# Kernel optimization log

Hardware: AMD Instinct MI355X
Metric: run time of the kernel (lower is better)

Reference implementation:

```python
import jax, jax.numpy as jnp
import numpy as np

N, E, G = 20000, 320000, 128
H, TE, CD = 128, 128, 64
HEADS, DH = 4, 32          # inner = 128 == H
L = 6


def _fwd(p, edge_index, batch):
    """Faithful forward of CrystalDiffusionModel (eval mode: dropout = identity).
    EquivariantGraphConv (imported in the original) is implemented as the standard
    edge-conditioned message-passing conv: m_ij = silu(W[h_src; h_dst; e_ij] + b),
    agg = scatter_add over dst, h' = W_u[h; agg] + b_u."""
    x, ea, t = p['x'], p['edge_attr'], p['t']
    n = x.shape[0]
    h = x @ p['Wn'] + p['bn']                      # [N,H] node embedding
    ef = ea @ p['We'] + p['be']                    # [E,H] edge embedding

    # sinusoidal time embedding -> MLP
    half = TE // 2
    freq = jnp.exp(-jnp.arange(half, dtype=jnp.float32) * (np.log(10000.0) / (half - 1)))
    te = t[:, None] * freq[None, :]
    te = jnp.concatenate([jnp.sin(te), jnp.cos(te)], axis=-1)          # [G,TE]
    te = jax.nn.silu(te @ p['tm_W1'] + p['tm_b1']) @ p['tm_W2'] + p['tm_b2']

    def mlp2(z, W1, b1, W2, b2):
        return jax.nn.silu(z @ W1 + b1) @ W2 + b2

    topo_e = mlp2(p['topo_cond'], p['topo_W1'], p['topo_b1'], p['topo_W2'], p['topo_b2'])
    stab_e = mlp2(p['stab_cond'], p['stab_W1'], p['stab_b1'], p['stab_W2'], p['stab_b2'])
    sust_e = mlp2(p['sust_cond'], p['sust_W1'], p['sust_b1'], p['sust_W2'], p['sust_b2'])
    cond = mlp2(jnp.concatenate([topo_e, stab_e, sust_e], axis=-1),
                p['comb_W1'], p['comb_b1'], p['comb_W2'], p['comb_b2'])  # [G,CD]

    ctx = cond[batch]                               # [N,CD] per-node condition
    # context is a single token per query -> k,v constant across layers
    k = (ctx @ p['Wk']).reshape(n, HEADS, DH)
    v = (ctx @ p['Wv']).reshape(n, HEADS, DH)
    ti = jax.nn.silu(te)[batch]                     # [N,H] time influence (dropout=id)

    src, dst = edge_index[0], edge_index[1]
    scale = DH ** -0.5
    for i in range(L):
        Wm, bm = p['gnn_Wm'][i], p['gnn_bm'][i]
        # split concat-GEMM to avoid materializing [E, 3H]
        m = jax.nn.silu(h[src] @ Wm[:H] + h[dst] @ Wm[H:2 * H] + ef @ Wm[2 * H:] + bm)
        agg = jax.ops.segment_sum(m, dst, num_segments=n)               # [N,H]
        Wu, bu = p['gnn_Wu'][i], p['gnn_bu'][i]
        hu = h @ Wu[:H] + agg @ Wu[H:] + bu
        # LayerNorm
        mu = hu.mean(-1, keepdims=True)
        var = hu.var(-1, keepdims=True)
        hu = (hu - mu) * jax.lax.rsqrt(var + 1e-5) * p['ln_g'][i] + p['ln_b'][i]
        # cross-attention; context length is 1 so softmax over j is exactly 1
        q = (hu @ p['Wq']).reshape(n, HEADS, DH)
        sim = jnp.einsum('nhd,nhd->nh', q, k) * scale                   # [N,heads]
        attn = jax.nn.softmax(sim[..., None], axis=-1)                  # == 1.0
        out = (attn * v).reshape(n, HEADS * DH)
        hu = out @ p['Wo'] + p['bo']
        h = h + hu + ti                              # residual + time influence

    node_pred = jax.nn.silu(h @ p['np_W1'] + p['np_b1']) @ p['np_W2'] + p['np_b2']
    pos_pred = jax.nn.silu(h @ p['pp_W1'] + p['pp_b1']) @ p['pp_W2'] + p['pp_b2']
    return node_pred, pos_pred


def setup_inputs() -> dict:
    key = jax.random.key(0)
    it = iter(jax.random.split(key, 96))

    def nrm(shape, s=0.02):
        return jax.random.normal(next(it), shape, jnp.float32) * s

    z = lambda *s: jnp.zeros(s, jnp.float32)
    inp = {
        'x': jax.random.normal(next(it), (N, 12), jnp.float32),
        'edge_index': jax.random.randint(next(it), (2, E), 0, N),
        'edge_attr': jax.random.normal(next(it), (E, 20), jnp.float32),
        'pos': jax.random.normal(next(it), (N, 3), jnp.float32),
        't': jax.random.uniform(next(it), (G,), jnp.float32) * 1000.0,
        'topo_cond': jax.random.normal(next(it), (G, 7), jnp.float32),
        'stab_cond': jax.random.normal(next(it), (G, 2), jnp.float32),
        'sust_cond': jax.random.normal(next(it), (G, 3), jnp.float32),
        'batch': jnp.sort(jax.random.randint(next(it), (N,), 0, G)),
        'Wn': nrm((12, H)), 'bn': z(H), 'We': nrm((20, H)), 'be': z(H),
        'tm_W1': nrm((TE, 2 * TE)), 'tm_b1': z(2 * TE), 'tm_W2': nrm((2 * TE, TE)), 'tm_b2': z(TE),
        'topo_W1': nrm((7, 32)), 'topo_b1': z(32), 'topo_W2': nrm((32, 32)), 'topo_b2': z(32),
        'stab_W1': nrm((2, 16)), 'stab_b1': z(16), 'stab_W2': nrm((16, 16)), 'stab_b2': z(16),
        'sust_W1': nrm((3, 16)), 'sust_b1': z(16), 'sust_W2': nrm((16, 16)), 'sust_b2': z(16),
        'comb_W1': nrm((64, CD)), 'comb_b1': z(CD), 'comb_W2': nrm((CD, CD)), 'comb_b2': z(CD),
        'Wq': nrm((H, HEADS * DH)), 'Wk': nrm((CD, HEADS * DH)), 'Wv': nrm((CD, HEADS * DH)),
        'Wo': nrm((HEADS * DH, H)), 'bo': z(H),
        'gnn_Wm': nrm((L, 3 * H, H)), 'gnn_bm': z(L, H),
        'gnn_Wu': nrm((L, 2 * H, H)), 'gnn_bu': z(L, H),
        'ln_g': jnp.ones((L, H), jnp.float32), 'ln_b': z(L, H),
        'np_W1': nrm((H, 2 * H)), 'np_b1': z(2 * H), 'np_W2': nrm((2 * H, 12)), 'np_b2': z(12),
        'pp_W1': nrm((H, H)), 'pp_b1': z(H), 'pp_W2': nrm((H, 3)), 'pp_b2': z(3),
    }
    return inp


def reference(x, edge_index, edge_attr, pos, t, topo_cond, stab_cond, sust_cond, batch,
              Wn, bn, We, be, tm_W1, tm_b1, tm_W2, tm_b2,
              topo_W1, topo_b1, topo_W2, topo_b2, stab_W1, stab_b1, stab_W2, stab_b2,
              sust_W1, sust_b1, sust_W2, sust_b2, comb_W1, comb_b1, comb_W2, comb_b2,
              Wq, Wk, Wv, Wo, bo, gnn_Wm, gnn_bm, gnn_Wu, gnn_bu, ln_g, ln_b,
              np_W1, np_b1, np_W2, np_b2, pp_W1, pp_b1, pp_W2, pp_b2):
    loc = dict(locals())
    p = {k: v for k, v in loc.items() if k not in ('edge_index', 'batch', 'pos')}
    return _fwd(p, edge_index, batch)
```

## Files before the change

kernel.cpp:

```cpp
#include <hip/hip_runtime.h>
#include <hip/hip_bf16.h>

#define NN 20000
#define GG 128

typedef __bf16 bf16x8_t __attribute__((ext_vector_type(8)));
typedef float  f32x4_t  __attribute__((ext_vector_type(4)));
typedef __hip_bfloat16 hbf16;

#define PK_NPW1 0
#define PK_PPW1 32768
#define PK_NPW2 49152
#define PK_PPW2 53248
#define PK_WN   55296
#define GADD_OFF 59392

__device__ __forceinline__ float silu_f(float v) {
    return v * __builtin_amdgcn_rcpf(1.0f + __expf(-v));
}

__device__ __forceinline__ void cp_async(hbf16* dst, const hbf16* src,
                                         int nbytes, int w, int lane) {
    const int per_wave = nbytes >> 2;
    const char* g = (const char*)src + w * per_wave + lane * 16;
    char* l = (char*)dst + w * per_wave + lane * 16;
    for (int j = 0; j < per_wave; j += 1024)
        __builtin_amdgcn_global_load_lds(
            (__attribute__((address_space(1))) void*)(g + j),
            (__attribute__((address_space(3))) void*)(l + j),
            16, 0, 0);
}

__global__ __launch_bounds__(512) void prep_kernel(
        const float* __restrict__ t, const float* __restrict__ topo,
        const float* __restrict__ stab, const float* __restrict__ sust,
        const float* __restrict__ tmW1, const float* __restrict__ tmb1,
        const float* __restrict__ tmW2, const float* __restrict__ tmb2,
        const float* __restrict__ topoW1, const float* __restrict__ topob1,
        const float* __restrict__ topoW2, const float* __restrict__ topob2,
        const float* __restrict__ stabW1, const float* __restrict__ stabb1,
        const float* __restrict__ stabW2, const float* __restrict__ stabb2,
        const float* __restrict__ sustW1, const float* __restrict__ sustb1,
        const float* __restrict__ sustW2, const float* __restrict__ sustb2,
        const float* __restrict__ combW1, const float* __restrict__ combb1,
        const float* __restrict__ combW2, const float* __restrict__ combb2,
        const float* __restrict__ Wv, const float* __restrict__ Wo,
        const float* __restrict__ bo,
        const float* __restrict__ npW1, const float* __restrict__ npW2,
        const float* __restrict__ ppW1, const float* __restrict__ ppW2,
        const float* __restrict__ Wn,
        float* __restrict__ gadd, hbf16* __restrict__ wsb) {
    const int tid = threadIdx.x;

    if (blockIdx.x >= GG) {
        const int s = (blockIdx.x - GG) * 512 + tid;
        if (s < 32768) {
            const int p = s;
            const int j = p & 7, l = (p >> 3) & 63, kb = (p >> 9) & 3, ct = p >> 11;
            const int k = kb * 32 + ((l >> 4) << 3) + j;
            const int n = ct * 16 + (l & 15);
            wsb[PK_NPW1 + p] = __float2bfloat16(npW1[k * 256 + n]);
        } else if (s < 49152) {
            const int p = s - 32768;
            const int j = p & 7, l = (p >> 3) & 63, kb = (p >> 9) & 3, ct = p >> 11;
            const int k = kb * 32 + ((l >> 4) << 3) + j;
            const int n = ct * 16 + (l & 15);
            wsb[PK_PPW1 + p] = __float2bfloat16(ppW1[k * 128 + n]);
        } else if (s < 53248) {
            const int p = s - 49152;
            const int j = p & 7, l = (p >> 3) & 63, kb = p >> 9;
            const int k = kb * 32 + ((l >> 4) << 3) + j;
            const int n = l & 15;
            wsb[PK_NPW2 + p] = __float2bfloat16(n < 12 ? npW2[k * 12 + n] : 0.0f);
        } else if (s < 55296) {
            const int p = s - 53248;
            const int j = p & 7, l = (p >> 3) & 63, kb = p >> 9;
            const int k = kb * 32 + ((l >> 4) << 3) + j;
            const int n = l & 15;
            wsb[PK_PPW2 + p] = __float2bfloat16(n < 3 ? ppW2[k * 3 + n] : 0.0f);
        } else if (s < 59392) {
            const int p = s - 55296;
            const int j = p & 7, l = (p >> 3) & 63, ct = p >> 9;
            const int k = ((l >> 4) << 3) + j;
            const int n = ct * 16 + (l & 15);
            wsb[PK_WN + p] = __float2bfloat16(k < 12 ? Wn[k * 128 + n] : 0.0f);
        }
        return;
    }

    __shared__ float s_te[128];
    __shared__ float s_th1[256];
    __shared__ float s_tef[128];
    __shared__ float s_l1[64];
    __shared__ float s_cat[64];
    __shared__ float s_c1[64];
    __shared__ float s_cond[64];
    __shared__ float s_v[128];
    __shared__ float s_red[512];

    const int g = blockIdx.x;

    if (tid < 128) {
        const float tval = t[g];
        const int i = tid & 63;
        const float fr = __expf(-(float)i * 0.14619587892025688f);
        const float arg = tval * fr;
        s_te[tid] = (tid < 64) ? sinf(arg) : cosf(arg);
    } else if (tid < 192) {
        const int c = tid - 128;
        if (c < 32) {
            float acc = topob1[c];
            for (int k = 0; k < 7; ++k)
                acc += topo[g * 7 + k] * topoW1[k * 32 + c];
            s_l1[c] = silu_f(acc);
        } else if (c < 48) {
            const int j = c - 32;
            float acc = stabb1[j];
            for (int k = 0; k < 2; ++k)
                acc += stab[g * 2 + k] * stabW1[k * 16 + j];
            s_l1[c] = silu_f(acc);
        } else {
            const int j = c - 48;
            float acc = sustb1[j];
            for (int k = 0; k < 3; ++k)
                acc += sust[g * 3 + k] * sustW1[k * 16 + j];
            s_l1[c] = silu_f(acc);
        }
    }
    __syncthreads();

    {
        const int col = tid & 255, half = tid >> 8;
        float acc = 0.0f;
#pragma unroll 32
        for (int kk = 0; kk < 64; ++kk) {
            const int k = half * 64 + kk;
            acc += s_te[k] * tmW1[k * 256 + col];
        }
        s_red[half * 256 + col] = acc;
    }
    __syncthreads();
    if (tid < 256)
        s_th1[tid] = silu_f(tmb1[tid] + s_red[tid] + s_red[256 + tid]);
    __syncthreads();

    {
        const int col = tid & 127, qt = tid >> 7;
        float acc = 0.0f;
#pragma unroll 32
        for (int kk = 0; kk < 64; ++kk) {
            const int k = qt * 64 + kk;
            acc += s_th1[k] * tmW2[k * 128 + col];
        }
        s_red[qt * 128 + col] = acc;
    }
    __syncthreads();
    if (tid < 128) {
        s_tef[tid] = tmb2[tid] + s_red[tid] + s_red[128 + tid] +
                     s_red[256 + tid] + s_red[384 + tid];
    } else if (tid < 192) {
        const int c = tid - 128;
        if (c < 32) {
            float acc = topob2[c];
            for (int k = 0; k < 32; ++k)
                acc += s_l1[k] * topoW2[k * 32 + c];
            s_cat[c] = acc;
        } else if (c < 48) {
            const int j = c - 32;
            float acc = stabb2[j];
            for (int k = 0; k < 16; ++k)
                acc += s_l1[32 + k] * stabW2[k * 16 + j];
            s_cat[c] = acc;
        } else {
            const int j = c - 48;
            float acc = sustb2[j];
            for (int k = 0; k < 16; ++k)
                acc += s_l1[48 + k] * sustW2[k * 16 + j];
            s_cat[c] = acc;
        }
    }
    __syncthreads();

    {
        const int col = tid & 63, part = tid >> 6;
        float acc = 0.0f;
#pragma unroll
        for (int kk = 0; kk < 8; ++kk) {
            const int k = part * 8 + kk;
            acc += s_cat[k] * combW1[k * 64 + col];
        }
        s_red[part * 64 + col] = acc;
    }
    __syncthreads();
    if (tid < 64) {
        float a = combb1[tid];
#pragma unroll
        for (int p = 0; p < 8; ++p) a += s_red[p * 64 + tid];
        s_c1[tid] = silu_f(a);
    }
    __syncthreads();

    {
        const int col = tid & 63, part = tid >> 6;
        float acc = 0.0f;
#pragma unroll
        for (int kk = 0; kk < 8; ++kk) {
            const int k = part * 8 + kk;
            acc += s_c1[k] * combW2[k * 64 + col];
        }
        s_red[part * 64 + col] = acc;
    }
    __syncthreads();
    if (tid < 64) {
        float a = combb2[tid];
#pragma unroll
        for (int p = 0; p < 8; ++p) a += s_red[p * 64 + tid];
        s_cond[tid] = a;
    }
    __syncthreads();

    {
        const int col = tid & 127, qt = tid >> 7;
        float acc = 0.0f;
#pragma unroll
        for (int kk = 0; kk < 16; ++kk) {
            const int k = qt * 16 + kk;
            acc += s_cond[k] * Wv[k * 128 + col];
        }
        s_red[qt * 128 + col] = acc;
    }
    __syncthreads();
    if (tid < 128)
        s_v[tid] = s_red[tid] + s_red[128 + tid] + s_red[256 + tid] + s_red[384 + tid];
    __syncthreads();

    {
        const int col = tid & 127, qt = tid >> 7;
        float acc = 0.0f;
#pragma unroll 32
        for (int kk = 0; kk < 32; ++kk) {
            const int k = qt * 32 + kk;
            acc += s_v[k] * Wo[k * 128 + col];
        }
        s_red[qt * 128 + col] = acc;
    }
    __syncthreads();
    if (tid < 128)
        gadd[g * 128 + tid] = 6.0f * (bo[tid] + s_red[tid] + s_red[128 + tid] +
                                      s_red[256 + tid] + s_red[384 + tid] +
                                      silu_f(s_tef[tid]));
}

#define NGS 6

__global__ __launch_bounds__(256) void node_kernel(
        const float* __restrict__ x, const int* __restrict__ batch,
        const float* __restrict__ bn,
        const float* __restrict__ npb1, const float* __restrict__ npb2,
        const float* __restrict__ ppb1, const float* __restrict__ ppb2,
        const float* __restrict__ gadd, const hbf16* __restrict__ wsb,
        float* __restrict__ out) {
    __shared__ __align__(16) hbf16 s_wA[8192];
    __shared__ __align__(16) hbf16 s_wB[8192];
    __shared__ __align__(16) hbf16 s_wn[4096];
    __shared__ __align__(16) hbf16 tbuf[4 * 16 * 264];
    __shared__ float s_gadd[NGS * 128];
    __shared__ float s_bias[528];

    const int tid  = threadIdx.x;
    const int nb   = blockIdx.x * 64;
    const int w    = tid >> 6;
    const int lane = tid & 63;
    const int q    = lane >> 4;
    const int r    = lane & 15;
    const int n16  = nb + w * 16;

    hbf16* wb = tbuf + w * (16 * 264);

    cp_async(s_wn, wsb + PK_WN, 8192, w, lane);
    cp_async(s_wA, wsb + PK_NPW1, 16384, w, lane);

    const int g0 = batch[nb];
    for (int i = tid; i < NGS * 128; i += 256) {
        int gr = g0 + (i >> 7);
        if (gr > GG - 1) gr = GG - 1;
        s_gadd[i] = gadd[gr * 128 + (i & 127)];
    }
    for (int i = tid; i < 528; i += 256) {
        float v;
        if (i < 128) v = bn[i];
        else if (i < 384) v = npb1[i - 128];
        else if (i < 396) v = npb2[i - 384];
        else if (i < 524) v = ppb1[i - 396];
        else if (i < 527) v = ppb2[i - 524];
        else v = 0.0f;
        s_bias[i] = v;
    }

    bf16x8_t Ax;
    {
        const int node = n16 + r;
        float xv[8];
#pragma unroll
        for (int j = 0; j < 8; ++j) xv[j] = 0.0f;
        if (node < NN) {
            if (q == 0) {
                const float4 a = *reinterpret_cast<const float4*>(x + node * 12);
                const float4 b = *reinterpret_cast<const float4*>(x + node * 12 + 4);
                xv[0] = a.x; xv[1] = a.y; xv[2] = a.z; xv[3] = a.w;
                xv[4] = b.x; xv[5] = b.y; xv[6] = b.z; xv[7] = b.w;
            } else if (q == 1) {
                const float4 a = *reinterpret_cast<const float4*>(x + node * 12 + 8);
                xv[0] = a.x; xv[1] = a.y; xv[2] = a.z; xv[3] = a.w;
            }
        }
#pragma unroll
        for (int j = 0; j < 8; ++j) {
            const hbf16 tv = __float2bfloat16(xv[j]);
            Ax[j] = *reinterpret_cast<const __bf16*>(&tv);
        }
    }
    int gidx[4];
#pragma unroll
    for (int i = 0; i < 4; ++i) {
        int gn = n16 + q * 4 + i;
        if (gn > NN - 1) gn = NN - 1;
        gidx[i] = batch[gn] - g0;
    }
    __syncthreads();

    bf16x8_t Ah[4];
    {
        f32x4_t hacc[8];
#pragma unroll
        for (int ct = 0; ct < 8; ++ct) {
            const bf16x8_t Bf = *reinterpret_cast<const bf16x8_t*>(
                &s_wn[(ct * 64 + lane) * 8]);
            hacc[ct] = __builtin_amdgcn_mfma_f32_16x16x32_bf16(
                Ax, Bf, (f32x4_t){0.f, 0.f, 0.f, 0.f}, 0, 0, 0);
        }
#pragma unroll
        for (int ct = 0; ct < 8; ++ct) {
            const int n = ct * 16 + r;
            const float bv = s_bias[n];
#pragma unroll
            for (int i = 0; i < 4; ++i) {
                const int gi = gidx[i];
                const float ga = (gi < NGS) ? s_gadd[gi * 128 + n]
                                            : gadd[(g0 + gi) * 128 + n];
                wb[(q * 4 + i) * 136 + n] = __float2bfloat16(hacc[ct][i] + bv + ga);
            }
        }
#pragma unroll
        for (int kb = 0; kb < 4; ++kb)
            Ah[kb] = *reinterpret_cast<const bf16x8_t*>(
                &wb[r * 136 + kb * 32 + q * 8]);
    }

    auto npL1_quad = [&](int cbase, const hbf16* sw) {
#pragma unroll
        for (int ci = 0; ci < 4; ++ci) {
            f32x4_t acc = (f32x4_t){0.f, 0.f, 0.f, 0.f};
#pragma unroll
            for (int kb = 0; kb < 4; ++kb) {
                const bf16x8_t Bf = *reinterpret_cast<const bf16x8_t*>(
                    &sw[((ci * 4 + kb) * 64 + lane) * 8]);
                acc = __builtin_amdgcn_mfma_f32_16x16x32_bf16(Ah[kb], Bf, acc, 0, 0, 0);
            }
            const int col = (cbase * 4 + ci) * 16 + r;
            const float b1 = s_bias[128 + col];
#pragma unroll
            for (int i = 0; i < 4; ++i)
                wb[(q * 4 + i) * 264 + col] = __float2bfloat16(silu_f(acc[i] + b1));
        }
    };
    auto ppL1_quad = [&](int cbase, const hbf16* sw) {
#pragma unroll
        for (int ci = 0; ci < 4; ++ci) {
            f32x4_t acc = (f32x4_t){0.f, 0.f, 0.f, 0.f};
#pragma unroll
            for (int kb = 0; kb < 4; ++kb) {
                const bf16x8_t Bf = *reinterpret_cast<const bf16x8_t*>(
                    &sw[((ci * 4 + kb) * 64 + lane) * 8]);
                acc = __builtin_amdgcn_mfma_f32_16x16x32_bf16(Ah[kb], Bf, acc, 0, 0, 0);
            }
            const int col = (cbase * 4 + ci) * 16 + r;
            const float b1 = s_bias[396 + col];
#pragma unroll
            for (int i = 0; i < 4; ++i)
                wb[(q * 4 + i) * 136 + col] = __float2bfloat16(silu_f(acc[i] + b1));
        }
    };

    cp_async(s_wB, wsb + PK_NPW1 + 8192, 16384, w, lane);
    npL1_quad(0, s_wA);
    __syncthreads();

    cp_async(s_wA, wsb + PK_NPW1 + 16384, 16384, w, lane);
    npL1_quad(1, s_wB);
    __syncthreads();

    cp_async(s_wB, wsb + PK_NPW1 + 24576, 16384, w, lane);
    npL1_quad(2, s_wA);
    __syncthreads();

    cp_async(s_wA, wsb + PK_NPW2, 8192, w, lane);
    npL1_quad(3, s_wB);
    __syncthreads();

    cp_async(s_wB, wsb + PK_PPW1, 16384, w, lane);
    {
        f32x4_t acc2 = (f32x4_t){0.f, 0.f, 0.f, 0.f};
#pragma unroll
        for (int kb = 0; kb < 8; ++kb) {
            const bf16x8_t Af = *reinterpret_cast<const bf16x8_t*>(
                &wb[r * 264 + kb * 32 + q * 8]);
            const bf16x8_t Bf = *reinterpret_cast<const bf16x8_t*>(
                &s_wA[(kb * 64 + lane) * 8]);
            acc2 = __builtin_amdgcn_mfma_f32_16x16x32_bf16(Af, Bf, acc2, 0, 0, 0);
        }
        if (r < 12) {
            const float b2 = s_bias[384 + r];
#pragma unroll
            for (int i = 0; i < 4; ++i) {
                const int gn = n16 + q * 4 + i;
                if (gn < NN) out[gn * 12 + r] = acc2[i] + b2;
            }
        }
    }
    __syncthreads();

    cp_async(s_wA, wsb + PK_PPW1 + 8192, 16384, w, lane);
    ppL1_quad(0, s_wB);
    __syncthreads();

    cp_async(s_wB, wsb + PK_PPW2, 4096, w, lane);
    ppL1_quad(1, s_wA);
    __syncthreads();

    {
        f32x4_t acc2 = (f32x4_t){0.f, 0.f, 0.f, 0.f};
#pragma unroll
        for (int kb = 0; kb < 4; ++kb) {
            const bf16x8_t Af = *reinterpret_cast<const bf16x8_t*>(
                &wb[r * 136 + kb * 32 + q * 8]);
            const bf16x8_t Bf = *reinterpret_cast<const bf16x8_t*>(
                &s_wB[(kb * 64 + lane) * 8]);
            acc2 = __builtin_amdgcn_mfma_f32_16x16x32_bf16(Af, Bf, acc2, 0, 0, 0);
        }
        if (r < 3) {
            const float b2 = s_bias[524 + r];
#pragma unroll
            for (int i = 0; i < 4; ++i) {
                const int gn = n16 + q * 4 + i;
                if (gn < NN) out[NN * 12 + gn * 3 + r] = acc2[i] + b2;
            }
        }
    }
}

extern "C" void kernel_launch(void* const* d_in, const int* in_sizes, int n_in,
                              void* d_out, int out_size, void* d_ws, size_t ws_size,
                              hipStream_t stream) {
    const float* x      = (const float*)d_in[0];
    const float* t      = (const float*)d_in[4];
    const float* topo   = (const float*)d_in[5];
    const float* stab   = (const float*)d_in[6];
    const float* sust   = (const float*)d_in[7];
    const int*   batch  = (const int*)d_in[8];
    const float* Wn     = (const float*)d_in[9];
    const float* bn     = (const float*)d_in[10];
    const float* tmW1   = (const float*)d_in[13];
    const float* tmb1   = (const float*)d_in[14];
    const float* tmW2   = (const float*)d_in[15];
    const float* tmb2   = (const float*)d_in[16];
    const float* topoW1 = (const float*)d_in[17];
    const float* topob1 = (const float*)d_in[18];
    const float* topoW2 = (const float*)d_in[19];
    const float* topob2 = (const float*)d_in[20];
    const float* stabW1 = (const float*)d_in[21];
    const float* stabb1 = (const float*)d_in[22];
    const float* stabW2 = (const float*)d_in[23];
    const float* stabb2 = (const float*)d_in[24];
    const float* sustW1 = (const float*)d_in[25];
    const float* sustb1 = (const float*)d_in[26];
    const float* sustW2 = (const float*)d_in[27];
    const float* sustb2 = (const float*)d_in[28];
    const float* combW1 = (const float*)d_in[29];
    const float* combb1 = (const float*)d_in[30];
    const float* combW2 = (const float*)d_in[31];
    const float* combb2 = (const float*)d_in[32];
    const float* Wv     = (const float*)d_in[35];
    const float* Wo     = (const float*)d_in[36];
    const float* bo     = (const float*)d_in[37];
    const float* npW1   = (const float*)d_in[44];
    const float* npb1   = (const float*)d_in[45];
    const float* npW2   = (const float*)d_in[46];
    const float* npb2   = (const float*)d_in[47];
    const float* ppW1   = (const float*)d_in[48];
    const float* ppb1   = (const float*)d_in[49];
    const float* ppW2   = (const float*)d_in[50];
    const float* ppb2   = (const float*)d_in[51];

    hbf16* wsb = (hbf16*)d_ws;
    float* gadd = (float*)(wsb + GADD_OFF);
    float* out = (float*)d_out;

    prep_kernel<<<GG + 116, 512, 0, stream>>>(
        t, topo, stab, sust,
        tmW1, tmb1, tmW2, tmb2,
        topoW1, topob1, topoW2, topob2,
        stabW1, stabb1, stabW2, stabb2,
        sustW1, sustb1, sustW2, sustb2,
        combW1, combb1, combW2, combb2,
        Wv, Wo, bo,
        npW1, npW2, ppW1, ppW2, Wn,
        gadd, wsb);

    node_kernel<<<(NN + 63) / 64, 256, 0, stream>>>(
        x, batch, bn, npb1, npb2, ppb1, ppb2, gadd, wsb, out);
}
```

Before: 200.2 us.

## Use single-wave blocks that read packed weights directly from global memory

```diff
diff --git a/kernel.cpp b/kernel.cpp
--- a/kernel.cpp
+++ b/kernel.cpp
@@ -17,18 +17,6 @@
 
 __device__ __forceinline__ float silu_f(float v) {
     return v * __builtin_amdgcn_rcpf(1.0f + __expf(-v));
-}
-
-__device__ __forceinline__ void cp_async(hbf16* dst, const hbf16* src,
-                                         int nbytes, int w, int lane) {
-    const int per_wave = nbytes >> 2;
-    const char* g = (const char*)src + w * per_wave + lane * 16;
-    char* l = (char*)dst + w * per_wave + lane * 16;
-    for (int j = 0; j < per_wave; j += 1024)
-        __builtin_amdgcn_global_load_lds(
-            (__attribute__((address_space(1))) void*)(g + j),
-            (__attribute__((address_space(3))) void*)(l + j),
-            16, 0, 0);
 }
 
 __global__ __launch_bounds__(512) void prep_kernel(
@@ -251,51 +239,19 @@
                                       silu_f(s_tef[tid]));
 }
 
-#define NGS 6
-
-__global__ __launch_bounds__(256) void node_kernel(
+__global__ __launch_bounds__(64) void node_kernel(
         const float* __restrict__ x, const int* __restrict__ batch,
         const float* __restrict__ bn,
         const float* __restrict__ npb1, const float* __restrict__ npb2,
         const float* __restrict__ ppb1, const float* __restrict__ ppb2,
         const float* __restrict__ gadd, const hbf16* __restrict__ wsb,
         float* __restrict__ out) {
-    __shared__ __align__(16) hbf16 s_wA[8192];
-    __shared__ __align__(16) hbf16 s_wB[8192];
-    __shared__ __align__(16) hbf16 s_wn[4096];
-    __shared__ __align__(16) hbf16 tbuf[4 * 16 * 264];
-    __shared__ float s_gadd[NGS * 128];
-    __shared__ float s_bias[528];
-
-    const int tid  = threadIdx.x;
-    const int nb   = blockIdx.x * 64;
-    const int w    = tid >> 6;
-    const int lane = tid & 63;
+    __shared__ __align__(16) hbf16 wb[16 * 264];
+
+    const int lane = threadIdx.x;
     const int q    = lane >> 4;
     const int r    = lane & 15;
-    const int n16  = nb + w * 16;
-
-    hbf16* wb = tbuf + w * (16 * 264);
-
-    cp_async(s_wn, wsb + PK_WN, 8192, w, lane);
-    cp_async(s_wA, wsb + PK_NPW1, 16384, w, lane);
-
-    const int g0 = batch[nb];
-    for (int i = tid; i < NGS * 128; i += 256) {
-        int gr = g0 + (i >> 7);
-        if (gr > GG - 1) gr = GG - 1;
-        s_gadd[i] = gadd[gr * 128 + (i & 127)];
-    }
-    for (int i = tid; i < 528; i += 256) {
-        float v;
-        if (i < 128) v = bn[i];
-        else if (i < 384) v = npb1[i - 128];
-        else if (i < 396) v = npb2[i - 384];
-        else if (i < 524) v = ppb1[i - 396];
-        else if (i < 527) v = ppb2[i - 524];
-        else v = 0.0f;
-        s_bias[i] = v;
-    }
+    const int n16  = blockIdx.x * 16;
 
     bf16x8_t Ax;
     {
@@ -303,16 +259,14 @@
         float xv[8];
 #pragma unroll
         for (int j = 0; j < 8; ++j) xv[j] = 0.0f;
-        if (node < NN) {
-            if (q == 0) {
-                const float4 a = *reinterpret_cast<const float4*>(x + node * 12);
-                const float4 b = *reinterpret_cast<const float4*>(x + node * 12 + 4);
-                xv[0] = a.x; xv[1] = a.y; xv[2] = a.z; xv[3] = a.w;
-                xv[4] = b.x; xv[5] = b.y; xv[6] = b.z; xv[7] = b.w;
-            } else if (q == 1) {
-                const float4 a = *reinterpret_cast<const float4*>(x + node * 12 + 8);
-                xv[0] = a.x; xv[1] = a.y; xv[2] = a.z; xv[3] = a.w;
-            }
+        if (q == 0) {
+            const float4 a = *reinterpret_cast<const float4*>(x + node * 12);
+            const float4 b = *reinterpret_cast<const float4*>(x + node * 12 + 4);
+            xv[0] = a.x; xv[1] = a.y; xv[2] = a.z; xv[3] = a.w;
+            xv[4] = b.x; xv[5] = b.y; xv[6] = b.z; xv[7] = b.w;
+        } else if (q == 1) {
+            const float4 a = *reinterpret_cast<const float4*>(x + node * 12 + 8);
+            xv[0] = a.x; xv[1] = a.y; xv[2] = a.z; xv[3] = a.w;
         }
 #pragma unroll
         for (int j = 0; j < 8; ++j) {
@@ -320,14 +274,10 @@
             Ax[j] = *reinterpret_cast<const __bf16*>(&tv);
         }
     }
-    int gidx[4];
-#pragma unroll
-    for (int i = 0; i < 4; ++i) {
-        int gn = n16 + q * 4 + i;
-        if (gn > NN - 1) gn = NN - 1;
-        gidx[i] = batch[gn] - g0;
-    }
-    __syncthreads();
+    int gb[4];
+#pragma unroll
+    for (int i = 0; i < 4; ++i)
+        gb[i] = batch[n16 + q * 4 + i];
 
     bf16x8_t Ah[4];
     {
@@ -335,80 +285,45 @@
 #pragma unroll
         for (int ct = 0; ct < 8; ++ct) {
             const bf16x8_t Bf = *reinterpret_cast<const bf16x8_t*>(
-                &s_wn[(ct * 64 + lane) * 8]);
+                &wsb[PK_WN + (ct * 64 + lane) * 8]);
             hacc[ct] = __builtin_amdgcn_mfma_f32_16x16x32_bf16(
                 Ax, Bf, (f32x4_t){0.f, 0.f, 0.f, 0.f}, 0, 0, 0);
         }
 #pragma unroll
         for (int ct = 0; ct < 8; ++ct) {
             const int n = ct * 16 + r;
-            const float bv = s_bias[n];
-#pragma unroll
-            for (int i = 0; i < 4; ++i) {
-                const int gi = gidx[i];
-                const float ga = (gi < NGS) ? s_gadd[gi * 128 + n]
-                                            : gadd[(g0 + gi) * 128 + n];
-                wb[(q * 4 + i) * 136 + n] = __float2bfloat16(hacc[ct][i] + bv + ga);
-            }
-        }
+            const float bv = bn[n];
+#pragma unroll
+            for (int i = 0; i < 4; ++i)
+                wb[(q * 4 + i) * 136 + n] = __float2bfloat16(
+                    hacc[ct][i] + bv + gadd[gb[i] * 128 + n]);
+        }
+    }
+    __syncthreads();
+    {
 #pragma unroll
         for (int kb = 0; kb < 4; ++kb)
             Ah[kb] = *reinterpret_cast<const bf16x8_t*>(
                 &wb[r * 136 + kb * 32 + q * 8]);
     }
 
-    auto npL1_quad = [&](int cbase, const hbf16* sw) {
-#pragma unroll
-        for (int ci = 0; ci < 4; ++ci) {
-            f32x4_t acc = (f32x4_t){0.f, 0.f, 0.f, 0.f};
-#pragma unroll
-            for (int kb = 0; kb < 4; ++kb) {
-                const bf16x8_t Bf = *reinterpret_cast<const bf16x8_t*>(
-                    &sw[((ci * 4 + kb) * 64 + lane) * 8]);
-                acc = __builtin_amdgcn_mfma_f32_16x16x32_bf16(Ah[kb], Bf, acc, 0, 0, 0);
-            }
-            const int col = (cbase * 4 + ci) * 16 + r;
-            const float b1 = s_bias[128 + col];
-#pragma unroll
-            for (int i = 0; i < 4; ++i)
-                wb[(q * 4 + i) * 264 + col] = __float2bfloat16(silu_f(acc[i] + b1));
-        }
-    };
-    auto ppL1_quad = [&](int cbase, const hbf16* sw) {
-#pragma unroll
-        for (int ci = 0; ci < 4; ++ci) {
-            f32x4_t acc = (f32x4_t){0.f, 0.f, 0.f, 0.f};
-#pragma unroll
-            for (int kb = 0; kb < 4; ++kb) {
-                const bf16x8_t Bf = *reinterpret_cast<const bf16x8_t*>(
-                    &sw[((ci * 4 + kb) * 64 + lane) * 8]);
-                acc = __builtin_amdgcn_mfma_f32_16x16x32_bf16(Ah[kb], Bf, acc, 0, 0, 0);
-            }
-            const int col = (cbase * 4 + ci) * 16 + r;
-            const float b1 = s_bias[396 + col];
-#pragma unroll
-            for (int i = 0; i < 4; ++i)
-                wb[(q * 4 + i) * 136 + col] = __float2bfloat16(silu_f(acc[i] + b1));
-        }
-    };
-
-    cp_async(s_wB, wsb + PK_NPW1 + 8192, 16384, w, lane);
-    npL1_quad(0, s_wA);
-    __syncthreads();
-
-    cp_async(s_wA, wsb + PK_NPW1 + 16384, 16384, w, lane);
-    npL1_quad(1, s_wB);
-    __syncthreads();
-
-    cp_async(s_wB, wsb + PK_NPW1 + 24576, 16384, w, lane);
-    npL1_quad(2, s_wA);
-    __syncthreads();
-
-    cp_async(s_wA, wsb + PK_NPW2, 8192, w, lane);
-    npL1_quad(3, s_wB);
-    __syncthreads();
-
-    cp_async(s_wB, wsb + PK_PPW1, 16384, w, lane);
+#pragma unroll
+    for (int ct = 0; ct < 16; ++ct) {
+        f32x4_t acc = (f32x4_t){0.f, 0.f, 0.f, 0.f};
+#pragma unroll
+        for (int kb = 0; kb < 4; ++kb) {
+            const bf16x8_t Bf = *reinterpret_cast<const bf16x8_t*>(
+                &wsb[PK_NPW1 + ((ct * 4 + kb) * 64 + lane) * 8]);
+            acc = __builtin_amdgcn_mfma_f32_16x16x32_bf16(Ah[kb], Bf, acc, 0, 0, 0);
+        }
+        const int col = ct * 16 + r;
+        const float b1 = npb1[col];
+#pragma unroll
+        for (int i = 0; i < 4; ++i)
+            wb[(q * 4 + i) * 264 + col] = __float2bfloat16(silu_f(acc[i] + b1));
+    }
+    __syncthreads();
+
     {
         f32x4_t acc2 = (f32x4_t){0.f, 0.f, 0.f, 0.f};
 #pragma unroll
@@ -416,26 +331,33 @@
             const bf16x8_t Af = *reinterpret_cast<const bf16x8_t*>(
                 &wb[r * 264 + kb * 32 + q * 8]);
             const bf16x8_t Bf = *reinterpret_cast<const bf16x8_t*>(
-                &s_wA[(kb * 64 + lane) * 8]);
+                &wsb[PK_NPW2 + (kb * 64 + lane) * 8]);
             acc2 = __builtin_amdgcn_mfma_f32_16x16x32_bf16(Af, Bf, acc2, 0, 0, 0);
         }
         if (r < 12) {
-            const float b2 = s_bias[384 + r];
-#pragma unroll
-            for (int i = 0; i < 4; ++i) {
-                const int gn = n16 + q * 4 + i;
-                if (gn < NN) out[gn * 12 + r] = acc2[i] + b2;
-            }
-        }
-    }
-    __syncthreads();
-
-    cp_async(s_wA, wsb + PK_PPW1 + 8192, 16384, w, lane);
-    ppL1_quad(0, s_wB);
-    __syncthreads();
-
-    cp_async(s_wB, wsb + PK_PPW2, 4096, w, lane);
-    ppL1_quad(1, s_wA);
+            const float b2 = npb2[r];
+#pragma unroll
+            for (int i = 0; i < 4; ++i)
+                out[(n16 + q * 4 + i) * 12 + r] = acc2[i] + b2;
+        }
+    }
+    __syncthreads();
+
+#pragma unroll
+    for (int ct = 0; ct < 8; ++ct) {
+        f32x4_t acc = (f32x4_t){0.f, 0.f, 0.f, 0.f};
+#pragma unroll
+        for (int kb = 0; kb < 4; ++kb) {
+            const bf16x8_t Bf = *reinterpret_cast<const bf16x8_t*>(
+                &wsb[PK_PPW1 + ((ct * 4 + kb) * 64 + lane) * 8]);
+            acc = __builtin_amdgcn_mfma_f32_16x16x32_bf16(Ah[kb], Bf, acc, 0, 0, 0);
+        }
+        const int col = ct * 16 + r;
+        const float b1 = ppb1[col];
+#pragma unroll
+        for (int i = 0; i < 4; ++i)
+            wb[(q * 4 + i) * 136 + col] = __float2bfloat16(silu_f(acc[i] + b1));
+    }
     __syncthreads();
 
     {
@@ -445,16 +367,14 @@
             const bf16x8_t Af = *reinterpret_cast<const bf16x8_t*>(
                 &wb[r * 136 + kb * 32 + q * 8]);
             const bf16x8_t Bf = *reinterpret_cast<const bf16x8_t*>(
-                &s_wB[(kb * 64 + lane) * 8]);
+                &wsb[PK_PPW2 + (kb * 64 + lane) * 8]);
             acc2 = __builtin_amdgcn_mfma_f32_16x16x32_bf16(Af, Bf, acc2, 0, 0, 0);
         }
         if (r < 3) {
-            const float b2 = s_bias[524 + r];
-#pragma unroll
-            for (int i = 0; i < 4; ++i) {
-                const int gn = n16 + q * 4 + i;
-                if (gn < NN) out[NN * 12 + gn * 3 + r] = acc2[i] + b2;
-            }
+            const float b2 = ppb2[r];
+#pragma unroll
+            for (int i = 0; i < 4; ++i)
+                out[NN * 12 + (n16 + q * 4 + i) * 3 + r] = acc2[i] + b2;
         }
     }
 }
@@ -517,6 +437,6 @@
         npW1, npW2, ppW1, ppW2, Wn,
         gadd, wsb);
 
-    node_kernel<<<(NN + 63) / 64, 256, 0, stream>>>(
+    node_kernel<<<NN / 16, 64, 0, stream>>>(
         x, batch, bn, npb1, npb2, ppb1, ppb2, gadd, wsb, out);
 }
```

After: 187.5 us, median of 2. 6.3% less time.
